# Kernel optimization log

Measured on AMD Instinct MI355X. Metric: run time of the kernel, lower is better.

Reference implementation:

```python
import jax, jax.numpy as jnp
import numpy as np


def _hadamard_mats():
    r1 = np.array([[1,0,0,0,1,0,0,0],[0,1,0,0,0,1,0,0],[0,0,1,0,0,0,1,0],[0,0,0,1,0,0,0,1],[1,0,0,0,-1,0,0,0],[0,1,0,0,0,-1,0,0],[0,0,1,0,0,0,-1,0],[0,0,0,1,0,0,0,-1]], dtype=np.float32)
    r2 = np.array([[1,0,1,0,0,0,0,0],[0,1,0,1,0,0,0,0],[1,0,-1,0,0,0,0,0],[0,1,0,-1,0,0,0,0],[0,0,0,0,1,0,1,0],[0,0,0,0,0,1,0,1],[0,0,0,0,1,0,-1,0],[0,0,0,0,0,1,0,-1]], dtype=np.float32)
    r3 = np.array([[1,1,0,0,0,0,0,0],[1,-1,0,0,0,0,0,0],[0,0,1,1,0,0,0,0],[0,0,1,-1,0,0,0,0],[0,0,0,0,1,1,0,0],[0,0,0,0,1,-1,0,0],[0,0,0,0,0,0,1,1],[0,0,0,0,0,0,1,-1]], dtype=np.float32)
    lmul = r1.T @ r2.T @ r3.T  # l1.dot(l2).dot(l3)
    rmul = r1 @ r2 @ r3
    return jnp.asarray(lmul), jnp.asarray(rmul)


def setup_inputs() -> dict:
    key = jax.random.key(0)
    k1, k2 = jax.random.split(key)
    B, C, H, W = 16, 3, 512, 512
    inp = jax.random.normal(k1, (B, C, H, W), dtype=jnp.float32)
    lab = jax.random.normal(k2, (B, C, H, W), dtype=jnp.float32)
    lmul, rmul = _hadamard_mats()
    return {"input": inp, "label": lab, "lmul": lmul, "rmul": rmul}


def reference(input, label, lmul, rmul):
    B, C, H, W = input.shape
    diff = input - label
    # split into non-overlapping 8x8 blocks: [B, C, H//8, 8, W//8, 8]
    d = diff.reshape(B, C, H // 8, 8, W // 8, 8)
    # per-block: lmul @ block @ rmul
    t = jnp.einsum('ij,bchjwk,kl->bchiwl', lmul, d, rmul)
    return jnp.mean(jnp.abs(t))
```

## Files before the change

### kernel.cpp

```cpp
#include <hip/hip_runtime.h>


#define N_TOTAL ((float)(16LL * 3 * 512 * 512))
#define GRID1 1536

__global__ __launch_bounds__(256) void satd_partial(const float* __restrict__ a,
                                                    const float* __restrict__ b,
                                                    float* __restrict__ ws) {
    const int lane = threadIdx.x & 63;
    const int wid  = threadIdx.x >> 6;
    const int s    = blockIdx.x * 4 + wid;
    const int xh   = s & 1;
    const int y8   = (s >> 1) & 63;
    const int img  = s >> 7;

    const size_t base = (size_t)img * (512 * 512)
                      + (size_t)(y8 * 8) * 512 + (size_t)(xh * 256) + (lane << 2);

    float4 av[8], bv[8];
#pragma unroll
    for (int i = 0; i < 8; ++i) {
        av[i] = *reinterpret_cast<const float4*>(a + base + (size_t)(i * 512));
        bv[i] = *reinterpret_cast<const float4*>(b + base + (size_t)(i * 512));
    }

    float v[8][4];
#pragma unroll
    for (int r = 0; r < 8; ++r) {
        v[r][0] = av[r].x - bv[r].x;
        v[r][1] = av[r].y - bv[r].y;
        v[r][2] = av[r].z - bv[r].z;
        v[r][3] = av[r].w - bv[r].w;
    }

    const float sx = (lane & 1) ? -1.0f : 1.0f;
#pragma unroll
    for (int r = 0; r < 8; ++r)
#pragma unroll
        for (int c = 0; c < 4; ++c) {
            float p = __shfl_xor(v[r][c], 1);
            v[r][c] = fmaf(sx, v[r][c], p);
        }

#pragma unroll
    for (int r = 0; r < 8; ++r) {
        float u0 = v[r][0], u1 = v[r][1], u2 = v[r][2], u3 = v[r][3];
        float t0 = u0 + u2, t2 = u0 - u2, t1 = u1 + u3, t3 = u1 - u3;
        v[r][0] = t0 + t1; v[r][1] = t0 - t1;
        v[r][2] = t2 + t3; v[r][3] = t2 - t3;
    }

    float acc = 0.0f;
#pragma unroll
    for (int c = 0; c < 4; ++c) {
        float x0 = v[0][c], x1 = v[1][c], x2 = v[2][c], x3 = v[3][c];
        float x4 = v[4][c], x5 = v[5][c], x6 = v[6][c], x7 = v[7][c];
        float y0 = x0 + x4, y4 = x0 - x4, y1 = x1 + x5, y5 = x1 - x5;
        float y2 = x2 + x6, y6 = x2 - x6, y3 = x3 + x7, y7 = x3 - x7;
        float z0 = y0 + y2, z2 = y0 - y2, z1 = y1 + y3, z3 = y1 - y3;
        float z4 = y4 + y6, z6 = y4 - y6, z5 = y5 + y7, z7 = y5 - y7;
        acc += fabsf(z0 + z1) + fabsf(z0 - z1) + fabsf(z2 + z3) + fabsf(z2 - z3)
             + fabsf(z4 + z5) + fabsf(z4 - z5) + fabsf(z6 + z7) + fabsf(z6 - z7);
    }

#pragma unroll
    for (int off = 32; off >= 1; off >>= 1) acc += __shfl_down(acc, off);

    __shared__ float red[4];
    if (lane == 0) red[wid] = acc;
    __syncthreads();
    if (threadIdx.x == 0)
        ws[blockIdx.x] = red[0] + red[1] + red[2] + red[3];
}

__global__ __launch_bounds__(64) void satd_final(const float* __restrict__ ws,
                                                 float* __restrict__ out) {
    const int t = threadIdx.x;
    float s_ = 0.0f;
#pragma unroll
    for (int k = 0; k < GRID1 / 64; ++k) s_ += ws[t + 64 * k];

#pragma unroll
    for (int off = 32; off >= 1; off >>= 1) s_ += __shfl_down(s_, off);

    if (t == 0) out[0] = s_ * (1.0f / N_TOTAL);
}

extern "C" void kernel_launch(void* const* d_in, const int* in_sizes, int n_in,
                              void* d_out, int out_size, void* d_ws, size_t ws_size,
                              hipStream_t stream) {
    const float* a = (const float*)d_in[0];
    const float* b = (const float*)d_in[1];
    float* out = (float*)d_out;
    float* ws  = (float*)d_ws;

    satd_partial<<<dim3(GRID1), dim3(256), 0, stream>>>(a, b, ws);
    satd_final<<<dim3(1), dim3(64), 0, stream>>>(ws, out);
}
```

Baseline: 22.52 us.

## Split each 8-row strip across two wavefronts with LDS exchange for column transform

Each 8x8 block row strip is now handled by two wavefronts, each loading four rows, doing the row transforms, then exchanging halves through shared memory so each computes half of the column butterfly outputs. The grid doubles and launch bounds request higher occupancy, aiming for more memory-level parallelism and fewer registers per thread. In exchange it adds an LDS round-trip, a block-wide barrier, and wave-uniform branching.

```diff
diff --git a/kernel.cpp b/kernel.cpp
--- a/kernel.cpp
+++ b/kernel.cpp
@@ -2,31 +2,34 @@
 
 
 #define N_TOTAL ((float)(16LL * 3 * 512 * 512))
-#define GRID1 1536
+#define GRID1 3072
 
-__global__ __launch_bounds__(256) void satd_partial(const float* __restrict__ a,
-                                                    const float* __restrict__ b,
-                                                    float* __restrict__ ws) {
+__global__ __launch_bounds__(256, 8) void satd_partial(const float* __restrict__ a,
+                                                       const float* __restrict__ b,
+                                                       float* __restrict__ ws) {
     const int lane = threadIdx.x & 63;
     const int wid  = threadIdx.x >> 6;
-    const int s    = blockIdx.x * 4 + wid;
+    const int pl   = wid >> 1;
+    const int h    = wid & 1;
+    const int s    = blockIdx.x * 2 + pl;
     const int xh   = s & 1;
     const int y8   = (s >> 1) & 63;
     const int img  = s >> 7;
 
     const size_t base = (size_t)img * (512 * 512)
-                      + (size_t)(y8 * 8) * 512 + (size_t)(xh * 256) + (lane << 2);
+                      + (size_t)(y8 * 8 + h * 4) * 512 + (size_t)(xh * 256)
+                      + (lane << 2);
 
-    float4 av[8], bv[8];
+    float4 av[4], bv[4];
 #pragma unroll
-    for (int i = 0; i < 8; ++i) {
+    for (int i = 0; i < 4; ++i) {
         av[i] = *reinterpret_cast<const float4*>(a + base + (size_t)(i * 512));
         bv[i] = *reinterpret_cast<const float4*>(b + base + (size_t)(i * 512));
     }
 
-    float v[8][4];
+    float v[4][4];
 #pragma unroll
-    for (int r = 0; r < 8; ++r) {
+    for (int r = 0; r < 4; ++r) {
         v[r][0] = av[r].x - bv[r].x;
         v[r][1] = av[r].y - bv[r].y;
         v[r][2] = av[r].z - bv[r].z;
@@ -35,7 +38,7 @@
 
     const float sx = (lane & 1) ? -1.0f : 1.0f;
 #pragma unroll
-    for (int r = 0; r < 8; ++r)
+    for (int r = 0; r < 4; ++r)
 #pragma unroll
         for (int c = 0; c < 4; ++c) {
             float p = __shfl_xor(v[r][c], 1);
@@ -43,24 +46,43 @@
         }
 
 #pragma unroll
-    for (int r = 0; r < 8; ++r) {
+    for (int r = 0; r < 4; ++r) {
         float u0 = v[r][0], u1 = v[r][1], u2 = v[r][2], u3 = v[r][3];
         float t0 = u0 + u2, t2 = u0 - u2, t1 = u1 + u3, t3 = u1 - u3;
         v[r][0] = t0 + t1; v[r][1] = t0 - t1;
         v[r][2] = t2 + t3; v[r][3] = t2 - t3;
     }
 
+    __shared__ float4 xch[2][8][64];
+#pragma unroll
+    for (int r = 0; r < 4; ++r)
+        xch[pl][h * 4 + r][lane] = make_float4(v[r][0], v[r][1], v[r][2], v[r][3]);
+    __syncthreads();
+
+    float o[4][4];
+#pragma unroll
+    for (int r = 0; r < 4; ++r) {
+        float4 q = xch[pl][(1 - h) * 4 + r][lane];
+        o[r][0] = q.x; o[r][1] = q.y; o[r][2] = q.z; o[r][3] = q.w;
+    }
+
     float acc = 0.0f;
 #pragma unroll
     for (int c = 0; c < 4; ++c) {
-        float x0 = v[0][c], x1 = v[1][c], x2 = v[2][c], x3 = v[3][c];
-        float x4 = v[4][c], x5 = v[5][c], x6 = v[6][c], x7 = v[7][c];
+        float x0, x1, x2, x3, x4, x5, x6, x7;
+        if (h == 0) { x0 = v[0][c]; x1 = v[1][c]; x2 = v[2][c]; x3 = v[3][c];
+                      x4 = o[0][c]; x5 = o[1][c]; x6 = o[2][c]; x7 = o[3][c]; }
+        else        { x0 = o[0][c]; x1 = o[1][c]; x2 = o[2][c]; x3 = o[3][c];
+                      x4 = v[0][c]; x5 = v[1][c]; x6 = v[2][c]; x7 = v[3][c]; }
         float y0 = x0 + x4, y4 = x0 - x4, y1 = x1 + x5, y5 = x1 - x5;
         float y2 = x2 + x6, y6 = x2 - x6, y3 = x3 + x7, y7 = x3 - x7;
-        float z0 = y0 + y2, z2 = y0 - y2, z1 = y1 + y3, z3 = y1 - y3;
-        float z4 = y4 + y6, z6 = y4 - y6, z5 = y5 + y7, z7 = y5 - y7;
-        acc += fabsf(z0 + z1) + fabsf(z0 - z1) + fabsf(z2 + z3) + fabsf(z2 - z3)
-             + fabsf(z4 + z5) + fabsf(z4 - z5) + fabsf(z6 + z7) + fabsf(z6 - z7);
+        if (h == 0) {
+            float z0 = y0 + y2, z2 = y0 - y2, z1 = y1 + y3, z3 = y1 - y3;
+            acc += fabsf(z0 + z1) + fabsf(z0 - z1) + fabsf(z2 + z3) + fabsf(z2 - z3);
+        } else {
+            float z4 = y4 + y6, z6 = y4 - y6, z5 = y5 + y7, z7 = y5 - y7;
+            acc += fabsf(z4 + z5) + fabsf(z4 - z5) + fabsf(z6 + z7) + fabsf(z6 - z7);
+        }
     }
 
 #pragma unroll
```

Measured after the change: 22.67 us. About the same (+0.7%).
